# Optimization experiments

Hardware: AMD Instinct MI355X
Metric: run time of the kernel (lower is better)

Reference implementation:

```python
import jax, jax.numpy as jnp
import numpy as np

N = 100000   # nodes
E = 1600000  # edges
D = 128      # emb_dim == in_dim
L = 5        # num_layer
G = 128      # graphs in batch
T = 10       # num_tasks
NB = 4       # edge (bond) types
BN_EPS = 1e-5


def setup_inputs() -> dict:
    key = jax.random.key(0)
    ks = jax.random.split(key, 10)
    x = jax.random.normal(ks[0], (N, D), jnp.float32)
    edge_index = jax.random.randint(ks[1], (2, E), 0, N, dtype=jnp.int32)
    edge_attr = jax.random.randint(ks[2], (E,), 0, NB, dtype=jnp.int32)
    batch = jnp.sort(jax.random.randint(ks[3], (N,), 0, G, dtype=jnp.int32))
    # stacked per-layer params (layer 0 has in_dim == emb_dim == D)
    W = jax.random.normal(ks[4], (L, D, D), jnp.float32) * 0.05
    b = jnp.zeros((L, D), jnp.float32)
    root = jax.random.normal(ks[5], (L, D), jnp.float32) * 0.05   # root_emb.weight per layer
    bond = jax.random.normal(ks[6], (L, NB, D), jnp.float32) * 0.05  # bond encoder tables
    gamma = jnp.ones((L, D), jnp.float32)
    beta = jnp.zeros((L, D), jnp.float32)
    W_out = jax.random.normal(ks[7], (D, T), jnp.float32) * 0.05
    b_out = jnp.zeros((T,), jnp.float32)
    return {"x": x, "edge_index": edge_index, "edge_attr": edge_attr, "batch": batch,
            "W": W, "b": b, "root": root, "bond": bond, "gamma": gamma, "beta": beta,
            "W_out": W_out, "b_out": b_out}


def reference(x, edge_index, edge_attr, batch, W, b, root, bond, gamma, beta, W_out, b_out):
    row, col = edge_index[0], edge_index[1]
    # degree of source nodes (+1 self), symmetric-ish norm as in GCNConv.forward
    deg = jax.ops.segment_sum(jnp.ones((E,), x.dtype), row, num_segments=N) + 1.0  # [N]
    dinv = deg ** -0.5  # never inf since deg >= 1
    norm = dinv[row] * dinv[col]  # [E]
    h = x
    for l in range(L):
        hx = h @ W[l] + b[l]                                   # [N, D] linear
        ee = bond[l][edge_attr]                                # [E, D] edge embedding gather
        msg = norm[:, None] * jax.nn.relu(hx[row] + ee)        # [E, D] message
        agg = jax.ops.segment_sum(msg, col, num_segments=N)    # [N, D] scatter-add to targets
        h2 = agg + jax.nn.relu(hx + root[l]) / deg[:, None]    # self/root term
        # BatchNorm1d (training-mode batch stats, biased variance)
        mu = h2.mean(axis=0)
        var = h2.var(axis=0)
        h2 = (h2 - mu) * jax.lax.rsqrt(var + BN_EPS) * gamma[l] + beta[l]
        h = jax.nn.relu(h2)
    # global mean pool over graphs
    cnt = jnp.maximum(jax.ops.segment_sum(jnp.ones((N,), h.dtype), batch, num_segments=G), 1.0)
    hg = jax.ops.segment_sum(h, batch, num_segments=G) / cnt[:, None]  # [G, D]
    return hg @ W_out + b_out  # [G, T]
```

## Files before the change

kernel.cpp:

```cpp
#include <hip/hip_runtime.h>
#include <hip/hip_fp16.h>
#include <math.h>

#define N_NODES 100000
#define N_EDGES 1600000
#define DIM     128
#define NLAYER  5
#define NGRAPH  128
#define NTASK   10
#define NBOND   4
#define BN_EPS  1e-5f

__global__ __launch_bounds__(256) void scan1_kernel(
    const int* __restrict__ cnt, int* __restrict__ excl, int* __restrict__ bsum,
    const int* __restrict__ cnt_row, float* __restrict__ deg, float* __restrict__ dinv) {
  __shared__ int s[256];
  int t = threadIdx.x;
  int i = blockIdx.x * 256 + t;
  if (i < N_NODES) {
    float d = (float)cnt_row[i] + 1.0f;
    deg[i] = d;
    dinv[i] = rsqrtf(d);
  }
  int v = (i < N_NODES) ? cnt[i] : 0;
  s[t] = v;
  __syncthreads();
  for (int off = 1; off < 256; off <<= 1) {
    int add = (t >= off) ? s[t - off] : 0;
    __syncthreads();
    s[t] += add;
    __syncthreads();
  }
  if (i < N_NODES) excl[i] = s[t] - v;
  if (t == 255) bsum[blockIdx.x] = s[255];
}

__global__ __launch_bounds__(512) void scan2_kernel(
    const int* __restrict__ bsum, int* __restrict__ bexcl, int nb) {
  __shared__ int s[512];
  int t = threadIdx.x;
  int v = (t < nb) ? bsum[t] : 0;
  s[t] = v;
  __syncthreads();
  for (int off = 1; off < 512; off <<= 1) {
    int add = (t >= off) ? s[t - off] : 0;
    __syncthreads();
    s[t] += add;
    __syncthreads();
  }
  if (t < nb) bexcl[t] = s[t] - v;
}

__global__ __launch_bounds__(256) void scan3_kernel(
    int* __restrict__ excl, const int* __restrict__ bexcl) {
  int i = blockIdx.x * 256 + threadIdx.x;
  if (i < N_NODES) excl[i] += bexcl[blockIdx.x];
  if (i == 0) excl[N_NODES] = N_EDGES;
}

__global__ __launch_bounds__(256) void scatter_kernel(
    const int* __restrict__ row, const int* __restrict__ col,
    const int* __restrict__ attr, const int* __restrict__ csr_off,
    int* __restrict__ pos, const float* __restrict__ dinv,
    int* __restrict__ src_pack, float* __restrict__ enorm) {
  int e = blockIdx.x * blockDim.x + threadIdx.x;
  int stride = gridDim.x * blockDim.x;
  for (; e < N_EDGES; e += stride) {
    int d = col[e];
    int s = row[e];
    int p = csr_off[d] + atomicAdd(&pos[d], 1);
    src_pack[p] = s | (attr[e] << 20);
    enorm[p] = dinv[s] * dinv[d];
  }
}

__device__ __forceinline__ void bn_coeff(float s, float q, float g, float b,
                                         float& sc, float& sh) {
  const float invN = 1.0f / (float)N_NODES;
  float mu = s * invN;
  float ex2 = q * invN;
  float var = ex2 - mu * mu;
  float inv = rsqrtf(var + BN_EPS);
  sc = g * inv;
  sh = fmaf(-mu, sc, b);
}

__device__ __forceinline__ void bn_coeff4(float4 s, float4 q, float4 g, float4 b,
                                          float4& sc, float4& sh) {
  bn_coeff(s.x, q.x, g.x, b.x, sc.x, sh.x);
  bn_coeff(s.y, q.y, g.y, b.y, sc.y, sh.y);
  bn_coeff(s.z, q.z, g.z, b.z, sc.z, sh.z);
  bn_coeff(s.w, q.w, g.w, b.w, sc.w, sh.w);
}

#define GBM 128
template<int USEACT>
__device__ __forceinline__ void gemm_body(
    const float* __restrict__ hin, const float* __restrict__ W,
    const float* __restrict__ bias, const float* __restrict__ bnprev,
    const float* __restrict__ gammaL, const float* __restrict__ betaL,
    uint2* __restrict__ hxh, float4* hs, float4* Ws, int bid) {
  int t = threadIdx.x;
  int cg = t & 15;
  int rg = t >> 4;
  int cr = rg & 3;
  int slot = t & 7;
  int srow = t >> 3;
  int sswz = slot ^ (srow & 3);
  int r0 = bid * GBM;
  if (r0 > N_NODES - GBM) r0 = N_NODES - GBM;

  const float4* hg = (const float4*)hin;
  const float4* wg = (const float4*)W;
  const float4* bs4 = (const float4*)bnprev;
  const float4* g4 = (const float4*)gammaL;
  const float4* b4 = (const float4*)betaL;

  float acc0[4][4], acc1[4][4];
  {
    float b0[4], b1[4];
#pragma unroll
    for (int j = 0; j < 4; j++) {
      b0[j] = bias[4 * cg + j];
      b1[j] = bias[64 + 4 * cg + j];
    }
#pragma unroll
    for (int i = 0; i < 4; i++)
#pragma unroll
      for (int j = 0; j < 4; j++) { acc0[i][j] = b0[j]; acc1[i][j] = b1[j]; }
  }

  float4 psc, psh;
  if (USEACT) {
    bn_coeff4(bs4[slot], bs4[32 + slot], g4[slot], b4[slot], psc, psh);
  }
  float4 ph0 = hg[(size_t)(r0 + srow) * 32 + slot];
  float4 ph1 = hg[(size_t)(r0 + srow + 64) * 32 + slot];
  float4 pw0 = wg[t];
  float4 pw1 = wg[512 + t];

#pragma unroll 1
  for (int p = 0; p < 4; ++p) {
    float4 v0 = ph0, v1 = ph1;
    if (USEACT) {
      v0.x = fmaxf(fmaf(v0.x, psc.x, psh.x), 0.f);
      v0.y = fmaxf(fmaf(v0.y, psc.y, psh.y), 0.f);
      v0.z = fmaxf(fmaf(v0.z, psc.z, psh.z), 0.f);
      v0.w = fmaxf(fmaf(v0.w, psc.w, psh.w), 0.f);
      v1.x = fmaxf(fmaf(v1.x, psc.x, psh.x), 0.f);
      v1.y = fmaxf(fmaf(v1.y, psc.y, psh.y), 0.f);
      v1.z = fmaxf(fmaf(v1.z, psc.z, psh.z), 0.f);
      v1.w = fmaxf(fmaf(v1.w, psc.w, psh.w), 0.f);
    }
    hs[srow * 8 + sswz] = v0;
    hs[(srow + 64) * 8 + sswz] = v1;
    Ws[t] = pw0;
    Ws[512 + t] = pw1;
    __syncthreads();
    if (p < 3) {
      if (USEACT) {
        bn_coeff4(bs4[(p + 1) * 8 + slot], bs4[32 + (p + 1) * 8 + slot],
                  g4[(p + 1) * 8 + slot], b4[(p + 1) * 8 + slot], psc, psh);
      }
      ph0 = hg[(size_t)(r0 + srow) * 32 + (p + 1) * 8 + slot];
      ph1 = hg[(size_t)(r0 + srow + 64) * 32 + (p + 1) * 8 + slot];
      pw0 = wg[(p + 1) * 1024 + t];
      pw1 = wg[(p + 1) * 1024 + 512 + t];
    }
#pragma unroll 1
    for (int k4 = 0; k4 < 8; k4++) {
      float4 w0[4], w1[4];
#pragma unroll
      for (int kk = 0; kk < 4; kk++) {
        w0[kk] = Ws[(k4 * 4 + kk) * 32 + cg];
        w1[kk] = Ws[(k4 * 4 + kk) * 32 + 16 + cg];
      }
      int soff = k4 ^ cr;
#pragma unroll
      for (int i = 0; i < 4; i++) {
        float4 hf = hs[(rg + 32 * i) * 8 + soff];
#pragma unroll
        for (int kk = 0; kk < 4; kk++) {
          float hv = ((const float*)&hf)[kk];
          acc0[i][0] = fmaf(hv, w0[kk].x, acc0[i][0]);
          acc0[i][1] = fmaf(hv, w0[kk].y, acc0[i][1]);
          acc0[i][2] = fmaf(hv, w0[kk].z, acc0[i][2]);
          acc0[i][3] = fmaf(hv, w0[kk].w, acc0[i][3]);
          acc1[i][0] = fmaf(hv, w1[kk].x, acc1[i][0]);
          acc1[i][1] = fmaf(hv, w1[kk].y, acc1[i][1]);
          acc1[i][2] = fmaf(hv, w1[kk].z, acc1[i][2]);
          acc1[i][3] = fmaf(hv, w1[kk].w, acc1[i][3]);
        }
      }
    }
    __syncthreads();
  }
#pragma unroll
  for (int i = 0; i < 4; i++) {
    int grow = r0 + rg + 32 * i;
    __half2 a01 = __floats2half2_rn(acc0[i][0], acc0[i][1]);
    __half2 a23 = __floats2half2_rn(acc0[i][2], acc0[i][3]);
    __half2 c01 = __floats2half2_rn(acc1[i][0], acc1[i][1]);
    __half2 c23 = __floats2half2_rn(acc1[i][2], acc1[i][3]);
    uint2 u0, u1;
    u0.x = __builtin_bit_cast(unsigned int, a01);
    u0.y = __builtin_bit_cast(unsigned int, a23);
    u1.x = __builtin_bit_cast(unsigned int, c01);
    u1.y = __builtin_bit_cast(unsigned int, c23);
    hxh[(size_t)grow * 32 + cg] = u0;
    hxh[(size_t)grow * 32 + 16 + cg] = u1;
  }
}

__global__ __launch_bounds__(512, 4) void gemm_kernel(
    const float* __restrict__ hin, const float* __restrict__ W,
    const float* __restrict__ bias, const float* __restrict__ bnprev,
    const float* __restrict__ gammaL, const float* __restrict__ betaL,
    uint2* __restrict__ hxh, float* __restrict__ bnzero) {
  __shared__ float4 hs[128 * 8];
  __shared__ float4 Ws[32 * 32];
  if (blockIdx.x == 0 && threadIdx.x < 256) bnzero[threadIdx.x] = 0.0f;
  gemm_body<1>(hin, W, bias, bnprev, gammaL, betaL, hxh, hs, Ws, blockIdx.x);
}

__global__ __launch_bounds__(512, 4) void gemm0_hist_kernel(
    const float* __restrict__ x, const float* __restrict__ W,
    const float* __restrict__ bias, uint2* __restrict__ hxh,
    float* __restrict__ bnzero,
    const int* __restrict__ row, const int* __restrict__ col,
    int* __restrict__ cnt_row, int* __restrict__ cnt_col, int gblocks) {
  __shared__ float4 hs[128 * 8];
  __shared__ float4 Ws[32 * 32];
  int t = threadIdx.x;
  if ((int)blockIdx.x >= gblocks) {
    int i = ((int)blockIdx.x - gblocks) * 512 + t;
    int stride = ((int)gridDim.x - gblocks) * 512;
    for (; i < N_EDGES; i += stride) {
      atomicAdd(&cnt_row[row[i]], 1);
      atomicAdd(&cnt_col[col[i]], 1);
    }
    return;
  }
  if (blockIdx.x == 0 && t < 256) bnzero[t] = 0.0f;
  gemm_body<0>(x, W, bias, nullptr, nullptr, nullptr, hxh, hs, Ws, blockIdx.x);
}

__global__ __launch_bounds__(256) void agg_kernel(
    const uint2* __restrict__ hxh, const int* __restrict__ csr_off,
    const int* __restrict__ src_pack, const float* __restrict__ enorm,
    const float* __restrict__ bond, const float* __restrict__ root,
    const float* __restrict__ deg, float* __restrict__ h2,
    float* __restrict__ bnbuf) {
  __shared__ float4 bondS[NBOND * 32];
  __shared__ float4 rootS[32];
  __shared__ float sbn[256];
  int t = threadIdx.x;
  if (t < NBOND * 32) bondS[t] = ((const float4*)bond)[t];
  if (t < 32) rootS[t] = ((const float4*)root)[t];
  sbn[t] = 0.0f;
  __syncthreads();

  int lane = t & 63;
  int laneq = lane & 31;
  int half = lane >> 5;
  int wid = t >> 6;
  int gw = blockIdx.x * 4 + wid;
  int nw = gridDim.x * 4;
  float4* h24 = (float4*)h2;

  float s0 = 0.f, s1 = 0.f, s2 = 0.f, s3 = 0.f;
  float q0 = 0.f, q1 = 0.f, q2 = 0.f, q3 = 0.f;
  for (int n = gw; n < N_NODES; n += nw) {
    int e0 = csr_off[n], e1 = csr_off[n + 1];
    float a0 = 0.f, a1 = 0.f, a2 = 0.f, a3 = 0.f;
    int e = e0 + half;
    for (; e + 6 < e1; e += 8) {
      int sp0 = src_pack[e];
      int sp1 = src_pack[e + 2];
      int sp2 = src_pack[e + 4];
      int sp3 = src_pack[e + 6];
      float nr0 = enorm[e];
      float nr1 = enorm[e + 2];
      float nr2 = enorm[e + 4];
      float nr3 = enorm[e + 6];
      uint2 u0 = hxh[(size_t)(sp0 & 0xFFFFF) * 32 + laneq];
      uint2 u1 = hxh[(size_t)(sp1 & 0xFFFFF) * 32 + laneq];
      uint2 u2 = hxh[(size_t)(sp2 & 0xFFFFF) * 32 + laneq];
      uint2 u3 = hxh[(size_t)(sp3 & 0xFFFFF) * 32 + laneq];
      float4 b0 = bondS[(sp0 >> 20) * 32 + laneq];
      float4 b1 = bondS[(sp1 >> 20) * 32 + laneq];
      float4 b2 = bondS[(sp2 >> 20) * 32 + laneq];
      float4 b3 = bondS[(sp3 >> 20) * 32 + laneq];
      float2 v0a = __half22float2(__builtin_bit_cast(__half2, u0.x));
      float2 v0b = __half22float2(__builtin_bit_cast(__half2, u0.y));
      float2 v1a = __half22float2(__builtin_bit_cast(__half2, u1.x));
      float2 v1b = __half22float2(__builtin_bit_cast(__half2, u1.y));
      float2 v2a = __half22float2(__builtin_bit_cast(__half2, u2.x));
      float2 v2b = __half22float2(__builtin_bit_cast(__half2, u2.y));
      float2 v3a = __half22float2(__builtin_bit_cast(__half2, u3.x));
      float2 v3b = __half22float2(__builtin_bit_cast(__half2, u3.y));
      a0 = fmaf(nr0, fmaxf(v0a.x + b0.x, 0.f), a0);
      a1 = fmaf(nr0, fmaxf(v0a.y + b0.y, 0.f), a1);
      a2 = fmaf(nr0, fmaxf(v0b.x + b0.z, 0.f), a2);
      a3 = fmaf(nr0, fmaxf(v0b.y + b0.w, 0.f), a3);
      a0 = fmaf(nr1, fmaxf(v1a.x + b1.x, 0.f), a0);
      a1 = fmaf(nr1, fmaxf(v1a.y + b1.y, 0.f), a1);
      a2 = fmaf(nr1, fmaxf(v1b.x + b1.z, 0.f), a2);
      a3 = fmaf(nr1, fmaxf(v1b.y + b1.w, 0.f), a3);
      a0 = fmaf(nr2, fmaxf(v2a.x + b2.x, 0.f), a0);
      a1 = fmaf(nr2, fmaxf(v2a.y + b2.y, 0.f), a1);
      a2 = fmaf(nr2, fmaxf(v2b.x + b2.z, 0.f), a2);
      a3 = fmaf(nr2, fmaxf(v2b.y + b2.w, 0.f), a3);
      a0 = fmaf(nr3, fmaxf(v3a.x + b3.x, 0.f), a0);
      a1 = fmaf(nr3, fmaxf(v3a.y + b3.y, 0.f), a1);
      a2 = fmaf(nr3, fmaxf(v3b.x + b3.z, 0.f), a2);
      a3 = fmaf(nr3, fmaxf(v3b.y + b3.w, 0.f), a3);
    }
    for (; e < e1; e += 2) {
      int sp = src_pack[e];
      float nrm = enorm[e];
      uint2 u = hxh[(size_t)(sp & 0xFFFFF) * 32 + laneq];
      float4 eb = bondS[(sp >> 20) * 32 + laneq];
      float2 va = __half22float2(__builtin_bit_cast(__half2, u.x));
      float2 vb = __half22float2(__builtin_bit_cast(__half2, u.y));
      a0 = fmaf(nrm, fmaxf(va.x + eb.x, 0.f), a0);
      a1 = fmaf(nrm, fmaxf(va.y + eb.y, 0.f), a1);
      a2 = fmaf(nrm, fmaxf(vb.x + eb.z, 0.f), a2);
      a3 = fmaf(nrm, fmaxf(vb.y + eb.w, 0.f), a3);
    }
    a0 += __shfl_xor(a0, 32, 64);
    a1 += __shfl_xor(a1, 32, 64);
    a2 += __shfl_xor(a2, 32, 64);
    a3 += __shfl_xor(a3, 32, 64);
    if (half == 0) {
      float inv = 1.0f / deg[n];
      uint2 u = hxh[(size_t)n * 32 + laneq];
      float2 va = __half22float2(__builtin_bit_cast(__half2, u.x));
      float2 vb = __half22float2(__builtin_bit_cast(__half2, u.y));
      float4 r = rootS[laneq];
      a0 += fmaxf(va.x + r.x, 0.f) * inv;
      a1 += fmaxf(va.y + r.y, 0.f) * inv;
      a2 += fmaxf(vb.x + r.z, 0.f) * inv;
      a3 += fmaxf(vb.y + r.w, 0.f) * inv;
      float4 o;
      o.x = a0; o.y = a1; o.z = a2; o.w = a3;
      h24[(size_t)n * 32 + laneq] = o;
      s0 += a0; s1 += a1; s2 += a2; s3 += a3;
      q0 += a0 * a0; q1 += a1 * a1; q2 += a2 * a2; q3 += a3 * a3;
    }
  }
  if (half == 0) {
    int f = 4 * laneq;
    atomicAdd(&sbn[f + 0], s0);
    atomicAdd(&sbn[f + 1], s1);
    atomicAdd(&sbn[f + 2], s2);
    atomicAdd(&sbn[f + 3], s3);
    atomicAdd(&sbn[128 + f + 0], q0);
    atomicAdd(&sbn[128 + f + 1], q1);
    atomicAdd(&sbn[128 + f + 2], q2);
    atomicAdd(&sbn[128 + f + 3], q3);
  }
  __syncthreads();
  atomicAdd(&bnbuf[t], sbn[t]);
}

__global__ __launch_bounds__(256) void pool_kernel(
    const float* __restrict__ h2, const int* __restrict__ batch,
    const float* __restrict__ bnlast, const float* __restrict__ gammaL,
    const float* __restrict__ betaL,
    float* __restrict__ pool, float* __restrict__ pcnt) {
  int t = threadIdx.x;
  int lane = t & 63;
  int wid = t >> 6;
  int gw = blockIdx.x * 4 + wid;
  int nw = gridDim.x * 4;
  int chunk = (N_NODES + nw - 1) / nw;
  int n0 = gw * chunk;
  int n1 = min(n0 + chunk, N_NODES);
  if (n0 >= N_NODES) return;
  const float2* h22 = (const float2*)h2;
  int f0 = 2 * lane, f1 = f0 + 1;
  float sc0, sh0, sc1, sh1;
  bn_coeff(bnlast[f0], bnlast[128 + f0], gammaL[f0], betaL[f0], sc0, sh0);
  bn_coeff(bnlast[f1], bnlast[128 + f1], gammaL[f1], betaL[f1], sc1, sh1);
  int curg = batch[n0];
  float a0 = 0.f, a1 = 0.f, c = 0.f;
  for (int n = n0; n < n1; n++) {
    int g = batch[n];
    if (g != curg) {
      atomicAdd(&pool[curg * DIM + f0], a0);
      atomicAdd(&pool[curg * DIM + f1], a1);
      if (lane == 0) atomicAdd(&pcnt[curg], c);
      a0 = a1 = c = 0.f;
      curg = g;
    }
    float2 v = h22[(size_t)n * 64 + lane];
    a0 += fmaxf(fmaf(v.x, sc0, sh0), 0.f);
    a1 += fmaxf(fmaf(v.y, sc1, sh1), 0.f);
    c += 1.0f;
  }
  atomicAdd(&pool[curg * DIM + f0], a0);
  atomicAdd(&pool[curg * DIM + f1], a1);
  if (lane == 0) atomicAdd(&pcnt[curg], c);
}

__global__ __launch_bounds__(256) void out_kernel(
    const float* __restrict__ pool, const float* __restrict__ pcnt,
    const float* __restrict__ Wout, const float* __restrict__ bout,
    float* __restrict__ out) {
  int idx = blockIdx.x * blockDim.x + threadIdx.x;
  if (idx >= NGRAPH * NTASK) return;
  int g = idx / NTASK, tt = idx % NTASK;
  float inv = 1.0f / fmaxf(pcnt[g], 1.0f);
  float acc = bout[tt];
  for (int d = 0; d < DIM; d++)
    acc = fmaf(pool[g * DIM + d] * inv, Wout[d * NTASK + tt], acc);
  out[idx] = acc;
}

extern "C" void kernel_launch(void* const* d_in, const int* in_sizes, int n_in,
                              void* d_out, int out_size, void* d_ws, size_t ws_size,
                              hipStream_t stream) {
  const float* x     = (const float*)d_in[0];
  const int*   eidx  = (const int*)d_in[1];
  const int*   row   = eidx;
  const int*   col   = eidx + N_EDGES;
  const int*   eattr = (const int*)d_in[2];
  const int*   batch = (const int*)d_in[3];
  const float* W     = (const float*)d_in[4];
  const float* b     = (const float*)d_in[5];
  const float* root  = (const float*)d_in[6];
  const float* bond  = (const float*)d_in[7];
  const float* gamma = (const float*)d_in[8];
  const float* beta  = (const float*)d_in[9];
  const float* Wout  = (const float*)d_in[10];
  const float* bout  = (const float*)d_in[11];
  float* out = (float*)d_out;

  char* w = (char*)d_ws;
  size_t off = 0;
  auto alloc = [&](size_t bytes) -> void* {
    void* p = w + off;
    off = (off + bytes + 511) & ~(size_t)511;
    return p;
  };
  int*   cnt_row = (int*)alloc(N_NODES * 4);
  int*   cnt_col = (int*)alloc(N_NODES * 4);
  int*   pos     = (int*)alloc(N_NODES * 4);
  float* pool    = (float*)alloc(NGRAPH * DIM * 4);
  float* pcnt    = (float*)alloc(NGRAPH * 4);
  size_t zbytes  = off;
  int*   csr     = (int*)alloc((N_NODES + 1) * 4);
  int*   bsum    = (int*)alloc(512 * 4);
  int*   bexcl   = (int*)alloc(512 * 4);
  float* deg     = (float*)alloc(N_NODES * 4);
  float* dinv    = (float*)alloc(N_NODES * 4);
  int*   spck    = (int*)alloc((size_t)N_EDGES * 4);
  float* enorm   = (float*)alloc((size_t)N_EDGES * 4);
  uint2* hxh     = (uint2*)alloc((size_t)N_NODES * DIM * 2);
  float* hA      = (float*)alloc((size_t)N_NODES * DIM * 4);
  float* hB      = (float*)alloc((size_t)N_NODES * DIM * 4);
  float* bnbufA  = (float*)alloc(256 * 4);
  float* bnbufB  = (float*)alloc(256 * 4);

  hipMemsetAsync(d_ws, 0, zbytes, stream);

  const int gblocks = (N_NODES + GBM - 1) / GBM;
  gemm0_hist_kernel<<<gblocks + 512, 512, 0, stream>>>(
      x, W, b, hxh, bnbufA, row, col, cnt_row, cnt_col, gblocks);

  const int nb = (N_NODES + 255) / 256;
  scan1_kernel<<<nb, 256, 0, stream>>>(cnt_col, csr, bsum, cnt_row, deg, dinv);
  scan2_kernel<<<1, 512, 0, stream>>>(bsum, bexcl, nb);
  scan3_kernel<<<nb, 256, 0, stream>>>(csr, bexcl);
  scatter_kernel<<<2048, 256, 0, stream>>>(row, col, eattr, csr, pos, dinv, spck, enorm);

  agg_kernel<<<2048, 256, 0, stream>>>(
      hxh, csr, spck, enorm, bond, root, deg, hA, bnbufA);

  const float* hin = hA;
  for (int l = 1; l < NLAYER; l++) {
    float* h2      = (l % 2 == 0) ? hA : hB;
    float* bufcur  = (l % 2 == 0) ? bnbufA : bnbufB;
    float* bufprev = (l % 2 == 0) ? bnbufB : bnbufA;
    gemm_kernel<<<gblocks, 512, 0, stream>>>(
        hin, W + (size_t)l * DIM * DIM, b + l * DIM,
        bufprev, gamma + (size_t)(l - 1) * DIM, beta + (size_t)(l - 1) * DIM,
        hxh, bufcur);
    agg_kernel<<<2048, 256, 0, stream>>>(
        hxh, csr, spck, enorm, bond + (size_t)l * NBOND * DIM, root + l * DIM,
        deg, h2, bufcur);
    hin = h2;
  }
  pool_kernel<<<256, 256, 0, stream>>>(hin, batch, bnbufA,
                                       gamma + 4 * DIM, beta + 4 * DIM, pool, pcnt);
  out_kernel<<<5, 256, 0, stream>>>(pool, pcnt, Wout, bout, out);
}
```

Baseline: 1.222 ms.

## Replace FP32 FMA GEMM with FP16 MFMA and pre-converted half weights

The per-layer node linear transform now runs on MFMA 16x16x32 f16 instructions instead of scalar FP32 FMAs. Each block stages a 64-row tile of activations as half precision in swizzled LDS. A new one-time kernel converts all layer weights into the MFMA B-fragment layout in FP16. This removes the compute-bound FP32 GEMM cost, but inputs are now rounded to half before the multiply, which may shift accuracy. The output stores are also now scalar half writes with a column-strided pattern.

```diff
diff --git a/kernel.cpp b/kernel.cpp
--- a/kernel.cpp
+++ b/kernel.cpp
@@ -10,6 +10,9 @@
 #define NTASK   10
 #define NBOND   4
 #define BN_EPS  1e-5f
+
+typedef __attribute__((ext_vector_type(8))) _Float16 half8;
+typedef __attribute__((ext_vector_type(4))) float f32x4;
 
 __global__ __launch_bounds__(256) void scan1_kernel(
     const int* __restrict__ cnt, int* __restrict__ excl, int* __restrict__ bsum,
@@ -85,164 +88,138 @@
   sh = fmaf(-mu, sc, b);
 }
 
-__device__ __forceinline__ void bn_coeff4(float4 s, float4 q, float4 g, float4 b,
-                                          float4& sc, float4& sh) {
-  bn_coeff(s.x, q.x, g.x, b.x, sc.x, sh.x);
-  bn_coeff(s.y, q.y, g.y, b.y, sc.y, sh.y);
-  bn_coeff(s.z, q.z, g.z, b.z, sc.z, sh.z);
-  bn_coeff(s.w, q.w, g.w, b.w, sc.w, sh.w);
-}
-
-#define GBM 128
+__global__ __launch_bounds__(256) void wcvt_kernel(
+    const float* __restrict__ W, uint4* __restrict__ W16) {
+  int g = (blockIdx.x * 256 + threadIdx.x) >> 6;
+  int lane = threadIdx.x & 63;
+  if (g >= NLAYER * 32) return;
+  int layer = g >> 5;
+  int rem = g & 31;
+  int kb = rem >> 3, ct = rem & 7;
+  const float* Wl = W + (size_t)layer * DIM * DIM;
+  int c = ct * 16 + (lane & 15);
+  int kbase = kb * 32 + (lane >> 4) * 8;
+  __half h[8];
+#pragma unroll
+  for (int e = 0; e < 8; e++)
+    h[e] = __float2half_rn(Wl[(size_t)(kbase + e) * DIM + c]);
+  uint4 u;
+  u.x = __builtin_bit_cast(unsigned int, __halves2half2(h[0], h[1]));
+  u.y = __builtin_bit_cast(unsigned int, __halves2half2(h[2], h[3]));
+  u.z = __builtin_bit_cast(unsigned int, __halves2half2(h[4], h[5]));
+  u.w = __builtin_bit_cast(unsigned int, __halves2half2(h[6], h[7]));
+  W16[(size_t)g * 64 + lane] = u;
+}
+
+#define GBM 64
 template<int USEACT>
 __device__ __forceinline__ void gemm_body(
-    const float* __restrict__ hin, const float* __restrict__ W,
+    const float* __restrict__ hin, const uint4* __restrict__ W16,
     const float* __restrict__ bias, const float* __restrict__ bnprev,
     const float* __restrict__ gammaL, const float* __restrict__ betaL,
-    uint2* __restrict__ hxh, float4* hs, float4* Ws, int bid) {
-  int t = threadIdx.x;
-  int cg = t & 15;
-  int rg = t >> 4;
-  int cr = rg & 3;
-  int slot = t & 7;
-  int srow = t >> 3;
-  int sswz = slot ^ (srow & 3);
+    __half* __restrict__ hxh, uint4* As, float* scS, float* shS, int bid) {
+  int t = threadIdx.x;
+  int lane = t & 63, w = t >> 6;
+  if (USEACT) {
+    if (t < 128) {
+      float sc, sh;
+      bn_coeff(bnprev[t], bnprev[128 + t], gammaL[t], betaL[t], sc, sh);
+      scS[t] = sc; shS[t] = sh;
+    }
+    __syncthreads();
+  }
   int r0 = bid * GBM;
   if (r0 > N_NODES - GBM) r0 = N_NODES - GBM;
 
   const float4* hg = (const float4*)hin;
-  const float4* wg = (const float4*)W;
-  const float4* bs4 = (const float4*)bnprev;
-  const float4* g4 = (const float4*)gammaL;
-  const float4* b4 = (const float4*)betaL;
-
-  float acc0[4][4], acc1[4][4];
-  {
-    float b0[4], b1[4];
-#pragma unroll
-    for (int j = 0; j < 4; j++) {
-      b0[j] = bias[4 * cg + j];
-      b1[j] = bias[64 + 4 * cg + j];
-    }
-#pragma unroll
-    for (int i = 0; i < 4; i++)
-#pragma unroll
-      for (int j = 0; j < 4; j++) { acc0[i][j] = b0[j]; acc1[i][j] = b1[j]; }
-  }
-
-  float4 psc, psh;
-  if (USEACT) {
-    bn_coeff4(bs4[slot], bs4[32 + slot], g4[slot], b4[slot], psc, psh);
-  }
-  float4 ph0 = hg[(size_t)(r0 + srow) * 32 + slot];
-  float4 ph1 = hg[(size_t)(r0 + srow + 64) * 32 + slot];
-  float4 pw0 = wg[t];
-  float4 pw1 = wg[512 + t];
-
-#pragma unroll 1
-  for (int p = 0; p < 4; ++p) {
-    float4 v0 = ph0, v1 = ph1;
+  int srow = t >> 2;
+#pragma unroll
+  for (int i = 0; i < 4; i++) {
+    int s = (t & 3) + 4 * i;
+    float4 a = hg[(size_t)(r0 + srow) * 32 + 2 * s];
+    float4 b = hg[(size_t)(r0 + srow) * 32 + 2 * s + 1];
     if (USEACT) {
-      v0.x = fmaxf(fmaf(v0.x, psc.x, psh.x), 0.f);
-      v0.y = fmaxf(fmaf(v0.y, psc.y, psh.y), 0.f);
-      v0.z = fmaxf(fmaf(v0.z, psc.z, psh.z), 0.f);
-      v0.w = fmaxf(fmaf(v0.w, psc.w, psh.w), 0.f);
-      v1.x = fmaxf(fmaf(v1.x, psc.x, psh.x), 0.f);
-      v1.y = fmaxf(fmaf(v1.y, psc.y, psh.y), 0.f);
-      v1.z = fmaxf(fmaf(v1.z, psc.z, psh.z), 0.f);
-      v1.w = fmaxf(fmaf(v1.w, psc.w, psh.w), 0.f);
-    }
-    hs[srow * 8 + sswz] = v0;
-    hs[(srow + 64) * 8 + sswz] = v1;
-    Ws[t] = pw0;
-    Ws[512 + t] = pw1;
-    __syncthreads();
-    if (p < 3) {
-      if (USEACT) {
-        bn_coeff4(bs4[(p + 1) * 8 + slot], bs4[32 + (p + 1) * 8 + slot],
-                  g4[(p + 1) * 8 + slot], b4[(p + 1) * 8 + slot], psc, psh);
-      }
-      ph0 = hg[(size_t)(r0 + srow) * 32 + (p + 1) * 8 + slot];
-      ph1 = hg[(size_t)(r0 + srow + 64) * 32 + (p + 1) * 8 + slot];
-      pw0 = wg[(p + 1) * 1024 + t];
-      pw1 = wg[(p + 1) * 1024 + 512 + t];
-    }
-#pragma unroll 1
-    for (int k4 = 0; k4 < 8; k4++) {
-      float4 w0[4], w1[4];
-#pragma unroll
-      for (int kk = 0; kk < 4; kk++) {
-        w0[kk] = Ws[(k4 * 4 + kk) * 32 + cg];
-        w1[kk] = Ws[(k4 * 4 + kk) * 32 + 16 + cg];
-      }
-      int soff = k4 ^ cr;
-#pragma unroll
-      for (int i = 0; i < 4; i++) {
-        float4 hf = hs[(rg + 32 * i) * 8 + soff];
-#pragma unroll
-        for (int kk = 0; kk < 4; kk++) {
-          float hv = ((const float*)&hf)[kk];
-          acc0[i][0] = fmaf(hv, w0[kk].x, acc0[i][0]);
-          acc0[i][1] = fmaf(hv, w0[kk].y, acc0[i][1]);
-          acc0[i][2] = fmaf(hv, w0[kk].z, acc0[i][2]);
-          acc0[i][3] = fmaf(hv, w0[kk].w, acc0[i][3]);
-          acc1[i][0] = fmaf(hv, w1[kk].x, acc1[i][0]);
-          acc1[i][1] = fmaf(hv, w1[kk].y, acc1[i][1]);
-          acc1[i][2] = fmaf(hv, w1[kk].z, acc1[i][2]);
-          acc1[i][3] = fmaf(hv, w1[kk].w, acc1[i][3]);
-        }
-      }
-    }
-    __syncthreads();
-  }
-#pragma unroll
-  for (int i = 0; i < 4; i++) {
-    int grow = r0 + rg + 32 * i;
-    __half2 a01 = __floats2half2_rn(acc0[i][0], acc0[i][1]);
-    __half2 a23 = __floats2half2_rn(acc0[i][2], acc0[i][3]);
-    __half2 c01 = __floats2half2_rn(acc1[i][0], acc1[i][1]);
-    __half2 c23 = __floats2half2_rn(acc1[i][2], acc1[i][3]);
-    uint2 u0, u1;
-    u0.x = __builtin_bit_cast(unsigned int, a01);
-    u0.y = __builtin_bit_cast(unsigned int, a23);
-    u1.x = __builtin_bit_cast(unsigned int, c01);
-    u1.y = __builtin_bit_cast(unsigned int, c23);
-    hxh[(size_t)grow * 32 + cg] = u0;
-    hxh[(size_t)grow * 32 + 16 + cg] = u1;
-  }
-}
-
-__global__ __launch_bounds__(512, 4) void gemm_kernel(
-    const float* __restrict__ hin, const float* __restrict__ W,
+      int k = s * 8;
+      a.x = fmaxf(fmaf(a.x, scS[k],     shS[k]),     0.f);
+      a.y = fmaxf(fmaf(a.y, scS[k + 1], shS[k + 1]), 0.f);
+      a.z = fmaxf(fmaf(a.z, scS[k + 2], shS[k + 2]), 0.f);
+      a.w = fmaxf(fmaf(a.w, scS[k + 3], shS[k + 3]), 0.f);
+      b.x = fmaxf(fmaf(b.x, scS[k + 4], shS[k + 4]), 0.f);
+      b.y = fmaxf(fmaf(b.y, scS[k + 5], shS[k + 5]), 0.f);
+      b.z = fmaxf(fmaf(b.z, scS[k + 6], shS[k + 6]), 0.f);
+      b.w = fmaxf(fmaf(b.w, scS[k + 7], shS[k + 7]), 0.f);
+    }
+    uint4 u;
+    u.x = __builtin_bit_cast(unsigned int, __floats2half2_rn(a.x, a.y));
+    u.y = __builtin_bit_cast(unsigned int, __floats2half2_rn(a.z, a.w));
+    u.z = __builtin_bit_cast(unsigned int, __floats2half2_rn(b.x, b.y));
+    u.w = __builtin_bit_cast(unsigned int, __floats2half2_rn(b.z, b.w));
+    As[srow * 16 + (s ^ (srow & 7))] = u;
+  }
+  __syncthreads();
+
+  f32x4 acc[8];
+#pragma unroll
+  for (int ct = 0; ct < 8; ct++) {
+    float bv = bias[ct * 16 + (lane & 15)];
+    f32x4 v; v[0] = bv; v[1] = bv; v[2] = bv; v[3] = bv;
+    acc[ct] = v;
+  }
+
+  int rl = w * 16 + (lane & 15);
+#pragma unroll
+  for (int kb = 0; kb < 4; kb++) {
+    int s = kb * 4 + (lane >> 4);
+    half8 af = __builtin_bit_cast(half8, As[rl * 16 + (s ^ (rl & 7))]);
+#pragma unroll
+    for (int ct = 0; ct < 8; ct++) {
+      half8 bf = __builtin_bit_cast(half8, W16[(kb * 8 + ct) * 64 + lane]);
+      acc[ct] = __builtin_amdgcn_mfma_f32_16x16x32_f16(af, bf, acc[ct], 0, 0, 0);
+    }
+  }
+
+  int colb = lane & 15;
+  int rowb = r0 + w * 16 + (lane >> 4) * 4;
+#pragma unroll
+  for (int ct = 0; ct < 8; ct++) {
+#pragma unroll
+    for (int reg = 0; reg < 4; reg++) {
+      hxh[(size_t)(rowb + reg) * 128 + ct * 16 + colb] = __float2half_rn(acc[ct][reg]);
+    }
+  }
+}
+
+__global__ __launch_bounds__(256) void gemm_kernel(
+    const float* __restrict__ hin, const uint4* __restrict__ W16,
     const float* __restrict__ bias, const float* __restrict__ bnprev,
     const float* __restrict__ gammaL, const float* __restrict__ betaL,
-    uint2* __restrict__ hxh, float* __restrict__ bnzero) {
-  __shared__ float4 hs[128 * 8];
-  __shared__ float4 Ws[32 * 32];
-  if (blockIdx.x == 0 && threadIdx.x < 256) bnzero[threadIdx.x] = 0.0f;
-  gemm_body<1>(hin, W, bias, bnprev, gammaL, betaL, hxh, hs, Ws, blockIdx.x);
-}
-
-__global__ __launch_bounds__(512, 4) void gemm0_hist_kernel(
-    const float* __restrict__ x, const float* __restrict__ W,
-    const float* __restrict__ bias, uint2* __restrict__ hxh,
+    __half* __restrict__ hxh, float* __restrict__ bnzero) {
+  __shared__ uint4 As[64 * 16];
+  __shared__ float scS[DIM], shS[DIM];
+  if (blockIdx.x == 0) bnzero[threadIdx.x] = 0.0f;
+  gemm_body<1>(hin, W16, bias, bnprev, gammaL, betaL, hxh, As, scS, shS, blockIdx.x);
+}
+
+__global__ __launch_bounds__(256) void gemm0_hist_kernel(
+    const float* __restrict__ x, const uint4* __restrict__ W16,
+    const float* __restrict__ bias, __half* __restrict__ hxh,
     float* __restrict__ bnzero,
     const int* __restrict__ row, const int* __restrict__ col,
     int* __restrict__ cnt_row, int* __restrict__ cnt_col, int gblocks) {
-  __shared__ float4 hs[128 * 8];
-  __shared__ float4 Ws[32 * 32];
+  __shared__ uint4 As[64 * 16];
+  __shared__ float scS[DIM], shS[DIM];
   int t = threadIdx.x;
   if ((int)blockIdx.x >= gblocks) {
-    int i = ((int)blockIdx.x - gblocks) * 512 + t;
-    int stride = ((int)gridDim.x - gblocks) * 512;
+    int i = ((int)blockIdx.x - gblocks) * 256 + t;
+    int stride = ((int)gridDim.x - gblocks) * 256;
     for (; i < N_EDGES; i += stride) {
       atomicAdd(&cnt_row[row[i]], 1);
       atomicAdd(&cnt_col[col[i]], 1);
     }
     return;
   }
-  if (blockIdx.x == 0 && t < 256) bnzero[t] = 0.0f;
-  gemm_body<0>(x, W, bias, nullptr, nullptr, nullptr, hxh, hs, Ws, blockIdx.x);
+  if (blockIdx.x == 0) bnzero[t] = 0.0f;
+  gemm_body<0>(x, W16, bias, nullptr, nullptr, nullptr, hxh, As, scS, shS, blockIdx.x);
 }
 
 __global__ __launch_bounds__(256) void agg_kernel(
@@ -460,14 +437,17 @@
   uint2* hxh     = (uint2*)alloc((size_t)N_NODES * DIM * 2);
   float* hA      = (float*)alloc((size_t)N_NODES * DIM * 4);
   float* hB      = (float*)alloc((size_t)N_NODES * DIM * 4);
+  uint4* W16     = (uint4*)alloc((size_t)NLAYER * 2048 * 16);
   float* bnbufA  = (float*)alloc(256 * 4);
   float* bnbufB  = (float*)alloc(256 * 4);
 
   hipMemsetAsync(d_ws, 0, zbytes, stream);
 
+  wcvt_kernel<<<40, 256, 0, stream>>>(W, W16);
+
   const int gblocks = (N_NODES + GBM - 1) / GBM;
-  gemm0_hist_kernel<<<gblocks + 512, 512, 0, stream>>>(
-      x, W, b, hxh, bnbufA, row, col, cnt_row, cnt_col, gblocks);
+  gemm0_hist_kernel<<<gblocks + 1024, 256, 0, stream>>>(
+      x, W16, b, (__half*)hxh, bnbufA, row, col, cnt_row, cnt_col, gblocks);
 
   const int nb = (N_NODES + 255) / 256;
   scan1_kernel<<<nb, 256, 0, stream>>>(cnt_col, csr, bsum, cnt_row, deg, dinv);
@@ -483,10 +463,10 @@
     float* h2      = (l % 2 == 0) ? hA : hB;
     float* bufcur  = (l % 2 == 0) ? bnbufA : bnbufB;
     float* bufprev = (l % 2 == 0) ? bnbufB : bnbufA;
-    gemm_kernel<<<gblocks, 512, 0, stream>>>(
-        hin, W + (size_t)l * DIM * DIM, b + l * DIM,
+    gemm_kernel<<<gblocks, 256, 0, stream>>>(
+        hin, W16 + (size_t)l * 2048, b + l * DIM,
         bufprev, gamma + (size_t)(l - 1) * DIM, beta + (size_t)(l - 1) * DIM,
-        hxh, bufcur);
+        (__half*)hxh, bufcur);
     agg_kernel<<<2048, 256, 0, stream>>>(
         hxh, csr, spck, enorm, bond + (size_t)l * NBOND * DIM, root + l * DIM,
         deg, h2, bufcur);
```

Result: faster. 1.057 ms (-13.5%).
